# Kernel optimization log

Hardware: AMD Instinct MI355X
Metric: run time of the kernel (lower is better)

Reference implementation:

```python
import jax, jax.numpy as jnp
import numpy as np

B, N, D, H, MLP = 4, 1024, 1024, 16, 4096  # seq_len N must equal dim D; D = H * dim_head
DH = D // H
EPS = 1e-5


def layernorm(x, g, b):
    mu = jnp.mean(x, axis=-1, keepdims=True)
    var = jnp.var(x, axis=-1, keepdims=True)
    return (x - mu) * jax.lax.rsqrt(var + EPS) * g + b


def setup_inputs() -> dict:
    key = jax.random.key(0)
    ks = jax.random.split(key, 12)
    s = 0.02
    return {
        "x": jax.random.normal(ks[0], (B, N, D), jnp.float32),
        "enc_out": jax.random.normal(ks[1], (B, N, D), jnp.float32),
        # SelfAttention (heads=1, dim_head=D); weights stored (in, out) so we apply x @ W
        "sa_wq": jax.random.normal(ks[2], (D, D), jnp.float32) * s,
        "sa_wk": jax.random.normal(ks[3], (D, D), jnp.float32) * s,
        "sa_wv": jax.random.normal(ks[4], (D, D), jnp.float32) * s,
        "sa_g": jnp.ones((D,), jnp.float32),
        "sa_b": jnp.zeros((D,), jnp.float32),
        # CrossAttention
        "ca_wq": jax.random.normal(ks[5], (D, D), jnp.float32) * s,
        "ca_wk": jax.random.normal(ks[6], (D, D), jnp.float32) * s,
        "ca_wv": jax.random.normal(ks[7], (D, D), jnp.float32) * s,
        "ca_g": jnp.ones((D,), jnp.float32),
        "ca_b": jnp.zeros((D,), jnp.float32),
        # FeedForward
        "w1": jax.random.normal(ks[8], (D, MLP), jnp.float32) * s,
        "b1": jnp.zeros((MLP,), jnp.float32),
        "w2": jax.random.normal(ks[9], (MLP, D), jnp.float32) * s,
        "b2": jnp.zeros((D,), jnp.float32),
        "ff_g": jnp.ones((D,), jnp.float32),
        "ff_b": jnp.zeros((D,), jnp.float32),
    }


def reference(x, enc_out, sa_wq, sa_wk, sa_wv, sa_g, sa_b,
              ca_wq, ca_wk, ca_wv, ca_g, ca_b,
              w1, b1, w2, b2, ff_g, ff_b):
    b, n, d = x.shape
    # --- SelfAttention: heads=1, dim_head=dim -> scale = dim**-0.5 ---
    sa_scale = 1.0 / jnp.sqrt(jnp.asarray(d, x.dtype))
    q = x @ sa_wq
    k = x @ sa_wk
    v = x @ sa_wv
    dots = jnp.einsum('bid,bjd->bij', q, k) * sa_scale
    attn = jax.nn.softmax(dots, axis=-1)
    sa = jnp.einsum('bij,bjd->bid', attn, v)
    sa = layernorm(sa + x, sa_g, sa_b)

    # --- CrossAttention: Q . (K K^T) before softmax ---
    dh = d // H
    ca_scale = 1.0 / jnp.sqrt(jnp.asarray(dh, x.dtype))
    qc = sa @ ca_wq                                     # [b, n, d]; broadcast over heads
    kc = (enc_out @ ca_wk).reshape(b, n, H, dh).transpose(0, 2, 1, 3)  # [b, h, n, dh]
    vc = (enc_out @ ca_wv).reshape(b, n, H, dh).transpose(0, 2, 1, 3)
    kkt = jnp.einsum('bhid,bhjd->bhij', kc, kc) * ca_scale             # [b, h, n, n]
    dots = jnp.einsum('bid,bhjd->bhij', qc, kkt) * ca_scale            # q's d contracts kkt's last dim (n == d)
    attn = jax.nn.softmax(dots, axis=-1)
    out = jnp.einsum('bhij,bhjd->bhid', attn, vc)
    out = out.transpose(0, 2, 1, 3).reshape(b, n, d)
    ca = layernorm(out + enc_out, ca_g, ca_b)

    # --- FeedForward (dropout = identity in eval) ---
    h = jax.nn.gelu(ca @ w1 + b1, approximate=False) @ w2 + b2
    return layernorm(h + ca, ff_g, ff_b)
```

## Files before the change

### kernel.cpp

```cpp
#include <hip/hip_runtime.h>
#include <math.h>
#include <stdint.h>

typedef unsigned short u16;
typedef u16   u16x8 __attribute__((ext_vector_type(8)));
typedef __bf16 bf16x8 __attribute__((ext_vector_type(8)));
typedef float  f32x4 __attribute__((ext_vector_type(4)));

#define B_   4
#define N_   1024
#define D_   1024
#define MLP_ 4096

__device__ __forceinline__ float bf2f(u16 v) {
    unsigned u = ((unsigned)v) << 16;
    return __builtin_bit_cast(float, u);
}
__device__ __forceinline__ u16 f2bf(float f) {
    unsigned u = __builtin_bit_cast(unsigned, f);
    u += 0x7fff + ((u >> 16) & 1);
    return (u16)(u >> 16);
}
__device__ __forceinline__ bf16x8 ld8(const u16* p) {
    return __builtin_bit_cast(bf16x8, *(const u16x8*)p);
}
__device__ __forceinline__ void gll16(const u16* g, u16* l) {
    __builtin_amdgcn_global_load_lds(
        (const __attribute__((address_space(1))) unsigned int*)g,
        (__attribute__((address_space(3))) unsigned int*)l,
        16, 0, 0);
}
__device__ __forceinline__ float gelu_f(float v) {
    float xs = v * 0.70710678118654752f;
    float ax = fabsf(xs);
    float t  = __builtin_amdgcn_rcpf(fmaf(0.3275911f, ax, 1.0f));
    float p  = fmaf(1.061405429f, t, -1.453152027f);
    p = fmaf(p, t, 1.421413741f);
    p = fmaf(p, t, -0.284496736f);
    p = fmaf(p, t, 0.254829592f);
    p *= t;
    float e = __expf(-ax * ax);
    float er = 1.0f - p * e;
    er = copysignf(er, xs);
    return 0.5f * v * (1.0f + er);
}

__global__ __launch_bounds__(256)
void prep_all(const float* __restrict__ x, const float* __restrict__ enc,
              u16* __restrict__ xB, u16* __restrict__ encB,
              const float* __restrict__ p0, const float* __restrict__ p1,
              const float* __restrict__ p2, const float* __restrict__ p3,
              const float* __restrict__ p4, const float* __restrict__ p5,
              u16* __restrict__ Wsa, u16* __restrict__ Wca)
{
    __shared__ u16 tile[32][33];
    int bid = blockIdx.x;
    if (bid < 4096) {
        const float* in = x; u16* out = xB;
        if (bid >= 2048) { in = enc; out = encB; bid -= 2048; }
        long i = (long)bid * 256 + threadIdx.x;
        f32x4 a = *(const f32x4*)&in[i * 8];
        f32x4 b = *(const f32x4*)&in[i * 8 + 4];
        u16x8 h;
        h[0] = f2bf(a[0]); h[1] = f2bf(a[1]); h[2] = f2bf(a[2]); h[3] = f2bf(a[3]);
        h[4] = f2bf(b[0]); h[5] = f2bf(b[1]); h[6] = f2bf(b[2]); h[7] = f2bf(b[3]);
        *(u16x8*)&out[i * 8] = h;
        return;
    }
    int sub = bid - 4096;
    const int z = sub >> 10;
    const int t2 = sub & 1023;
    const int bx = (t2 & 31) * 32, by = (t2 >> 5) * 32;
    const float* in = p0;
    if (z == 1) in = p1;
    else if (z == 2) in = p2;
    else if (z == 3) in = p3;
    else if (z == 4) in = p4;
    else if (z == 5) in = p5;
    u16* out = (z < 3) ? Wsa + (long)z * (1 << 20) : Wca + (long)(z - 3) * (1 << 20);
    const int tx = threadIdx.x & 31, ty = threadIdx.x >> 5;
#pragma unroll
    for (int i = ty; i < 32; i += 8)
        tile[i][tx] = f2bf(in[(long)(by + i) * 1024 + bx + tx]);
    __syncthreads();
#pragma unroll
    for (int i = ty; i < 32; i += 8)
        out[(long)(bx + i) * 1024 + by + tx] = tile[tx][i];
}

template<int TM, int TN, int BK, int OUTF32, int BIAS, int GELU>
__device__ __forceinline__ void gemm_body(
    const u16* __restrict__ A, const u16* __restrict__ Bt, char* __restrict__ Cp,
    const float* __restrict__ bias, float scale, int K,
    int lda, int ldb, int ldc, int m0, int n0)
{
    constexpr int MT = TM / 32, NT = TN / 32;
    constexpr int CPT = BK / 8;
    constexpr int RPP = 2048 / BK;
    constexpr int CMASK = (CPT - 1) & 7;
    __shared__ alignas(16) u16 As[2][TM * BK];
    __shared__ alignas(16) u16 Bs[2][TN * BK];
    const int t = threadIdx.x, lane = t & 63, w = t >> 6;
    const int wr = (w >> 1) * (TM / 2), wc = (w & 1) * (TN / 2);
    const int fr = lane & 15, fq = lane >> 4;
    f32x4 acc[MT][NT] = {};

    const int r0a = t / CPT;
    const int c0sw = ((t % CPT) ^ (r0a & CMASK)) * 8;
    auto stageA = [&](u16* dst, int k0) {
#pragma unroll
        for (int p = 0; p < TM / RPP; p++)
            gll16(A + (long)(m0 + p * RPP + r0a) * lda + k0 + c0sw, dst + p * 2048 + w * 512);
    };
    auto stageB = [&](u16* dst, int k0) {
#pragma unroll
        for (int p = 0; p < TN / RPP; p++)
            gll16(Bt + (long)(n0 + p * RPP + r0a) * ldb + k0 + c0sw, dst + p * 2048 + w * 512);
    };

    stageA(As[0], 0);
    stageB(Bs[0], 0);
    int cur = 0;
    for (int k0 = 0; k0 < K; k0 += BK) {
        __syncthreads();
        if (k0 + BK < K) {
            stageA(As[cur ^ 1], k0 + BK);
            stageB(Bs[cur ^ 1], k0 + BK);
        }
        const u16* as = As[cur];
        const u16* bs = Bs[cur];
#pragma unroll
        for (int kk = 0; kk < BK; kk += 32) {
            bf16x8 af[MT], bfv[NT];
#pragma unroll
            for (int mt = 0; mt < MT; mt++) {
                const int row = wr + mt * 16 + fr;
                af[mt] = ld8(&as[row * BK + ((((kk >> 3) + fq) ^ (row & CMASK)) << 3)]);
            }
#pragma unroll
            for (int nt = 0; nt < NT; nt++) {
                const int row = wc + nt * 16 + fr;
                bfv[nt] = ld8(&bs[row * BK + ((((kk >> 3) + fq) ^ (row & CMASK)) << 3)]);
            }
#pragma unroll
            for (int mt = 0; mt < MT; mt++)
#pragma unroll
                for (int nt = 0; nt < NT; nt++)
                    acc[mt][nt] = __builtin_amdgcn_mfma_f32_16x16x32_bf16(af[mt], bfv[nt], acc[mt][nt], 0, 0, 0);
        }
        cur ^= 1;
    }

#pragma unroll
    for (int nt = 0; nt < NT; nt++) {
        const int col = n0 + wc + nt * 16 + fr;
        float bv = 0.f;
        if (BIAS) bv = bias[col];
#pragma unroll
        for (int mt = 0; mt < MT; mt++) {
            const int rbase = m0 + wr + mt * 16 + fq * 4;
#pragma unroll
            for (int r = 0; r < 4; r++) {
                float v = acc[mt][nt][r] * scale;
                if (BIAS) v += bv;
                if (GELU) v = gelu_f(v);
                long idx = (long)(rbase + r) * ldc + col;
                if (OUTF32) ((float*)Cp)[idx] = v;
                else        ((u16*) Cp)[idx] = f2bf(v);
            }
        }
    }
}

template<int TM, int TN, int BK, int SEL, int OUTF32, int BIAS, int GELU>
__global__ __launch_bounds__(256, ((TM + TN >= 256) ? ((BK == 64) ? 2 : 4)
                                                    : ((BK == 64) ? 3 : 4)))
void gemm_a(const u16* __restrict__ A0, const u16* __restrict__ A1,
            const u16* __restrict__ B0, const u16* __restrict__ B1,
            void* __restrict__ C0v, void* __restrict__ C1v,
            const float* __restrict__ bias,
            float scale, int K,
            int lda, int ldb, int ldc,
            long sA, long sB, long sC)
{
    int by = blockIdx.y, bz = blockIdx.z;
    const u16* A = A0; const u16* Bt = B0; char* Cp = (char*)C0v;
    if (SEL == 1) {
        int half = gridDim.y >> 1;
        if (by >= half) { A = A1; Bt = B1; Cp = (char*)C1v; by -= half; }
    }
    A += bz * sA;  Bt += bz * sB;  Cp += bz * sC * (OUTF32 ? 4 : 2);
    gemm_body<TM, TN, BK, OUTF32, BIAS, GELU>(
        A, Bt, Cp, bias, scale, K, lda, ldb, ldc, blockIdx.x * TM, by * TN);
}

__global__ __launch_bounds__(256, 4)
void gemm_qkv4(const u16* __restrict__ xB,  const u16* __restrict__ Wq,
               const u16* __restrict__ Wk,  u16* __restrict__ qB,
               u16* __restrict__ kB,
               const u16* __restrict__ Wv,  const u16* __restrict__ Wvc,
               const u16* __restrict__ encB,
               u16* __restrict__ vTB, u16* __restrict__ vcTB)
{
    const long M1 = (long)N_ * D_;
    int bid = blockIdx.x;
    const u16* A; const u16* Bt; u16* C; int m0, n0;
    if (bid < 512) {
        int bx = bid & 31, by = bid >> 5;
        A = xB; m0 = bx * 128;
        if (by < 8) { Bt = Wq; C = qB; n0 = by * 128; }
        else        { Bt = Wk; C = kB; n0 = (by - 8) * 128; }
    } else {
        int sub = bid - 512;
        int bx = sub & 7, by = (sub >> 3) & 7, bz = sub >> 6;
        m0 = bx * 128; n0 = by * 128;
        if (bz < 4) { A = Wv;  Bt = xB   + (long)bz * M1;       C = vTB  + (long)bz * M1; }
        else        { A = Wvc; Bt = encB + (long)(bz - 4) * M1; C = vcTB + (long)(bz - 4) * M1; }
    }
    gemm_body<128, 128, 32, 0, 0, 0>(
        A, Bt, (char*)C, nullptr, 1.f, 1024, 1024, 1024, 1024, m0, n0);
}

template<int INF32>
__global__ __launch_bounds__(256)
void transpose_cast(const void* __restrict__ in, u16* __restrict__ out,
                    int R, int C, long sIn, long sOut)
{
    __shared__ u16 tile[32][33];
    const char* ip = (const char*)in + (long)blockIdx.z * sIn * (INF32 ? 4 : 2);
    u16*        op = out + (long)blockIdx.z * sOut;
    const int bx = blockIdx.x * 32, by = blockIdx.y * 32;
    const int tx = threadIdx.x & 31, ty = threadIdx.x >> 5;
#pragma unroll
    for (int i = ty; i < 32; i += 8) {
        long idx = (long)(by + i) * C + bx + tx;
        tile[i][tx] = INF32 ? f2bf(((const float*)ip)[idx]) : ((const u16*)ip)[idx];
    }
    __syncthreads();
#pragma unroll
    for (int i = ty; i < 32; i += 8) op[(long)(bx + i) * R + by + tx] = tile[tx][i];
}

__global__ __launch_bounds__(256)
void transpose_ff(const float* __restrict__ w1, const float* __restrict__ w2,
                  u16* __restrict__ o1, u16* __restrict__ o2)
{
    __shared__ u16 tile[32][33];
    const float* in; u16* out; int R, C, bx, by;
    if (blockIdx.z == 0) {
        in = w1; out = o1; R = 1024; C = 4096;
        bx = blockIdx.x; by = blockIdx.y;
    } else {
        in = w2; out = o2; R = 4096; C = 1024;
        bx = blockIdx.x >> 2; by = blockIdx.y * 4 + (blockIdx.x & 3);
    }
    const int x0 = bx * 32, y0 = by * 32;
    const int tx = threadIdx.x & 31, ty = threadIdx.x >> 5;
#pragma unroll
    for (int i = ty; i < 32; i += 8)
        tile[i][tx] = f2bf(in[(long)(y0 + i) * C + x0 + tx]);
    __syncthreads();
#pragma unroll
    for (int i = ty; i < 32; i += 8)
        out[(long)(x0 + i) * R + y0 + tx] = tile[tx][i];
}

__global__ __launch_bounds__(256)
void softmax_1024(const float* __restrict__ in, u16* __restrict__ out)
{
    const int lane = threadIdx.x & 63, wv = threadIdx.x >> 6;
    const long row = (long)blockIdx.x * 4 + wv;
    const float* p = in + row * 1024 + lane * 16;
    float v[16];
#pragma unroll
    for (int q = 0; q < 4; q++) {
        f32x4 a = *(const f32x4*)(p + q * 4);
#pragma unroll
        for (int e = 0; e < 4; e++) v[q * 4 + e] = a[e];
    }
    float mx = v[0];
#pragma unroll
    for (int i = 1; i < 16; i++) mx = fmaxf(mx, v[i]);
#pragma unroll
    for (int off = 32; off; off >>= 1) mx = fmaxf(mx, __shfl_xor(mx, off, 64));
    float s = 0.f;
#pragma unroll
    for (int i = 0; i < 16; i++) { v[i] = __expf(v[i] - mx); s += v[i]; }
#pragma unroll
    for (int off = 32; off; off >>= 1) s += __shfl_xor(s, off, 64);
    const float inv = 1.0f / s;
    u16* qp = out + row * 1024 + lane * 16;
#pragma unroll
    for (int q = 0; q < 2; q++) {
        u16x8 o;
#pragma unroll
        for (int e = 0; e < 8; e++) o[e] = f2bf(v[q * 8 + e] * inv);
        *(u16x8*)(qp + q * 8) = o;
    }
}

template<int AF32, int RESF32, int OUTF32>
__global__ __launch_bounds__(256)
void ln_res(const void* __restrict__ Av, const void* __restrict__ Rv,
            const float* __restrict__ g, const float* __restrict__ be,
            void* __restrict__ out)
{
    const int lane = threadIdx.x & 63, wv = threadIdx.x >> 6;
    const long row = (long)blockIdx.x * 4 + wv;
    const long off = row * 1024 + lane * 16;
    const int c0 = lane * 16;
    float v[16];
    if (AF32) {
#pragma unroll
        for (int q = 0; q < 4; q++) {
            f32x4 a = *((const f32x4*)((const float*)Av + off) + q);
#pragma unroll
            for (int e = 0; e < 4; e++) v[q * 4 + e] = a[e];
        }
    } else {
#pragma unroll
        for (int q = 0; q < 2; q++) {
            u16x8 a = *((const u16x8*)((const u16*)Av + off) + q);
#pragma unroll
            for (int e = 0; e < 8; e++) v[q * 8 + e] = bf2f(a[e]);
        }
    }
    if (RESF32) {
#pragma unroll
        for (int q = 0; q < 4; q++) {
            f32x4 a = *((const f32x4*)((const float*)Rv + off) + q);
#pragma unroll
            for (int e = 0; e < 4; e++) v[q * 4 + e] += a[e];
        }
    } else {
#pragma unroll
        for (int q = 0; q < 2; q++) {
            u16x8 a = *((const u16x8*)((const u16*)Rv + off) + q);
#pragma unroll
            for (int e = 0; e < 8; e++) v[q * 8 + e] += bf2f(a[e]);
        }
    }
    float s = 0.f;
#pragma unroll
    for (int i = 0; i < 16; i++) s += v[i];
#pragma unroll
    for (int o = 32; o; o >>= 1) s += __shfl_xor(s, o, 64);
    const float mu = s * (1.f / 1024.f);
    float s2 = 0.f;
#pragma unroll
    for (int i = 0; i < 16; i++) { float d = v[i] - mu; s2 += d * d; }
#pragma unroll
    for (int o = 32; o; o >>= 1) s2 += __shfl_xor(s2, o, 64);
    const float rs = rsqrtf(s2 * (1.f / 1024.f) + 1e-5f);

    float ov[16];
#pragma unroll
    for (int q = 0; q < 4; q++) {
        f32x4 gv = *(const f32x4*)&g[c0 + q * 4];
        f32x4 bv = *(const f32x4*)&be[c0 + q * 4];
#pragma unroll
        for (int e = 0; e < 4; e++)
            ov[q * 4 + e] = (v[q * 4 + e] - mu) * rs * gv[e] + bv[e];
    }
    if (OUTF32) {
#pragma unroll
        for (int q = 0; q < 4; q++) {
            f32x4 o;
#pragma unroll
            for (int e = 0; e < 4; e++) o[e] = ov[q * 4 + e];
            *((f32x4*)((float*)out + off) + q) = o;
        }
    } else {
#pragma unroll
        for (int q = 0; q < 2; q++) {
            u16x8 o;
#pragma unroll
            for (int e = 0; e < 8; e++) o[e] = f2bf(ov[q * 8 + e]);
            *((u16x8*)((u16*)out + off) + q) = o;
        }
    }
}

__global__ __launch_bounds__(256, 3)
void flash_ca(const u16* __restrict__ P, const u16* __restrict__ Kc,
              const u16* __restrict__ VT, u16* __restrict__ O)
{
    __shared__ alignas(16) u16 Ks[2][64 * 64];
    __shared__ alignas(16) u16 Vs[2][64 * 64];
    __shared__ alignas(16) u16 Ps[128 * 72];
    const int b = blockIdx.z, h = blockIdx.y, it = blockIdx.x;
    const long base = (long)b * N_ * D_;
    const int t = threadIdx.x, lane = t & 63, w = t >> 6;
    const int fr = lane & 15, fq = lane >> 4;

    bf16x8 qf[2][2];
#pragma unroll
    for (int mt = 0; mt < 2; mt++)
#pragma unroll
        for (int hf = 0; hf < 2; hf++)
            qf[mt][hf] = ld8(&P[base + (long)(it * 128 + w * 32 + mt * 16 + fr) * D_
                                + h * 64 + hf * 32 + fq * 8]);

    const int svr = t >> 3, svc = ((t & 7) ^ (svr & 7)) * 8;
    auto stageK = [&](int buf, int jt) {
#pragma unroll
        for (int p = 0; p < 2; p++)
            gll16(Kc + base + (long)(jt * 64 + p * 32 + svr) * D_ + h * 64 + svc,
                  &Ks[buf][p * 2048 + w * 512]);
    };
    auto stageV = [&](int buf, int jt) {
#pragma unroll
        for (int p = 0; p < 2; p++)
            gll16(VT + base + (long)(h * 64 + p * 32 + svr) * D_ + jt * 64 + svc,
                  &Vs[buf][p * 2048 + w * 512]);
    };

    f32x4 o[2][4] = {};
    float l_lane[2][4] = {};

    stageK(0, 0); stageV(0, 0);
    int cur = 0;
    for (int jt = 0; jt < 16; jt++) {
        __syncthreads();
        if (jt + 1 < 16) { stageK(cur ^ 1, jt + 1); stageV(cur ^ 1, jt + 1); }
        const u16* ks = Ks[cur];
        const u16* vs = Vs[cur];

        f32x4 st[2][4] = {};
        __builtin_amdgcn_s_setprio(1);
#pragma unroll
        for (int nt = 0; nt < 4; nt++) {
            const int row = nt * 16 + fr;
            bf16x8 b0 = ld8(&ks[row * 64 + ((fq ^ (row & 7)) << 3)]);
            bf16x8 b1 = ld8(&ks[row * 64 + (((fq + 4) ^ (row & 7)) << 3)]);
#pragma unroll
            for (int mt = 0; mt < 2; mt++) {
                st[mt][nt] = __builtin_amdgcn_mfma_f32_16x16x32_bf16(qf[mt][0], b0, st[mt][nt], 0, 0, 0);
                st[mt][nt] = __builtin_amdgcn_mfma_f32_16x16x32_bf16(qf[mt][1], b1, st[mt][nt], 0, 0, 0);
            }
        }
        __builtin_amdgcn_s_setprio(0);
#pragma unroll
        for (int mt = 0; mt < 2; mt++)
#pragma unroll
            for (int nt = 0; nt < 4; nt++)
#pragma unroll
                for (int r = 0; r < 4; r++) {
                    float e = __expf(st[mt][nt][r]);
                    l_lane[mt][r] += e;
                    Ps[(w * 32 + mt * 16 + fq * 4 + r) * 72 + nt * 16 + fr] = f2bf(e);
                }
        __asm__ volatile("s_waitcnt lgkmcnt(0)" ::: "memory");
        bf16x8 vf[4][2];
#pragma unroll
        for (int dt = 0; dt < 4; dt++) {
            const int row = dt * 16 + fr;
            vf[dt][0] = ld8(&vs[row * 64 + ((fq ^ (row & 7)) << 3)]);
            vf[dt][1] = ld8(&vs[row * 64 + (((fq + 4) ^ (row & 7)) << 3)]);
        }
        __builtin_amdgcn_s_setprio(1);
#pragma unroll
        for (int mt = 0; mt < 2; mt++) {
            bf16x8 p0 = ld8(&Ps[(w * 32 + mt * 16 + fr) * 72 + fq * 8]);
            bf16x8 p1 = ld8(&Ps[(w * 32 + mt * 16 + fr) * 72 + 32 + fq * 8]);
#pragma unroll
            for (int dt = 0; dt < 4; dt++) {
                o[mt][dt] = __builtin_amdgcn_mfma_f32_16x16x32_bf16(p0, vf[dt][0], o[mt][dt], 0, 0, 0);
                o[mt][dt] = __builtin_amdgcn_mfma_f32_16x16x32_bf16(p1, vf[dt][1], o[mt][dt], 0, 0, 0);
            }
        }
        __builtin_amdgcn_s_setprio(0);
        cur ^= 1;
    }
#pragma unroll
    for (int mt = 0; mt < 2; mt++)
#pragma unroll
        for (int r = 0; r < 4; r++) {
            float lt = l_lane[mt][r];
#pragma unroll
            for (int off = 1; off < 16; off <<= 1) lt += __shfl_xor(lt, off, 64);
            l_lane[mt][r] = 1.0f / lt;
        }
#pragma unroll
    for (int mt = 0; mt < 2; mt++)
#pragma unroll
        for (int dt = 0; dt < 4; dt++)
#pragma unroll
            for (int r = 0; r < 4; r++)
                O[base + (long)(it * 128 + w * 32 + mt * 16 + fq * 4 + r) * D_
                  + h * 64 + dt * 16 + fr] = f2bf(o[mt][dt][r] * l_lane[mt][r]);
}

extern "C" void kernel_launch(void* const* d_in, const int* in_sizes, int n_in,
                              void* d_out, int out_size, void* d_ws, size_t ws_size,
                              hipStream_t stream)
{
    const float* x     = (const float*)d_in[0];
    const float* enc   = (const float*)d_in[1];
    const float* sa_wq = (const float*)d_in[2];
    const float* sa_wk = (const float*)d_in[3];
    const float* sa_wv = (const float*)d_in[4];
    const float* sa_g  = (const float*)d_in[5];
    const float* sa_b  = (const float*)d_in[6];
    const float* ca_wq = (const float*)d_in[7];
    const float* ca_wk = (const float*)d_in[8];
    const float* ca_wv = (const float*)d_in[9];
    const float* ca_g  = (const float*)d_in[10];
    const float* ca_b  = (const float*)d_in[11];
    const float* w1    = (const float*)d_in[12];
    const float* b1    = (const float*)d_in[13];
    const float* w2    = (const float*)d_in[14];
    const float* b2    = (const float*)d_in[15];
    const float* ff_g  = (const float*)d_in[16];
    const float* ff_b  = (const float*)d_in[17];

    char* ws = (char*)d_ws;
    const size_t MB = 1ull << 20;
    u16*  xB    = (u16*)(ws + 0 * MB);
    u16*  attnB = (u16*)(ws + 0 * MB);
    u16*  w2T   = (u16*)(ws + 0 * MB);
    u16*  encB  = (u16*)(ws + 8 * MB);
    u16*  w1T   = (u16*)(ws + 8 * MB);
    u16*  Wsa   = (u16*)(ws + 16 * MB);
    u16*  Wca   = (u16*)(ws + 22 * MB);
    float* h2F  = (float*)(ws + 16 * MB);
    u16*  qBsa  = (u16*)(ws + 28 * MB);
    u16*  E     = (u16*)(ws + 28 * MB);
    u16*  kBsa  = (u16*)(ws + 36 * MB);
    u16*  qBca  = (u16*)(ws + 36 * MB);
    u16*  calnB = (u16*)(ws + 36 * MB);
    u16*  vTB   = (u16*)(ws + 44 * MB);
    u16*  kBca  = (u16*)(ws + 44 * MB);
    u16*  h1B   = (u16*)(ws + 44 * MB);
    u16*  vcTB  = (u16*)(ws + 52 * MB);
    float* scF  = (float*)(ws + 60 * MB);
    u16*  kcT   = (u16*)(ws + 60 * MB);

    const dim3 blk(256, 1, 1);
    const long M1 = (long)N_ * D_;
    const long W1M = (long)1024 * 1024;

    prep_all<<<dim3(10240, 1, 1), blk, 0, stream>>>(
        x, enc, xB, encB, sa_wq, sa_wk, sa_wv, ca_wq, ca_wk, ca_wv, Wsa, Wca);

    gemm_qkv4<<<dim3(1024, 1, 1), blk, 0, stream>>>(
        xB, Wsa, Wsa + W1M, qBsa, kBsa,
        Wsa + 2 * W1M, Wca + 2 * W1M, encB, vTB, vcTB);
    gemm_a<128,64,64,0,1,0,0><<<dim3(8, 16, 4), blk, 0, stream>>>(
        qBsa, nullptr, kBsa, nullptr, scF, nullptr, nullptr,
        0.03125f, 1024, 1024, 1024, 1024, M1, M1, M1);
    softmax_1024<<<dim3(1024, 1, 1), blk, 0, stream>>>(scF, attnB);
    gemm_a<128,64,64,0,1,0,0><<<dim3(8, 16, 4), blk, 0, stream>>>(
        attnB, nullptr, vTB, nullptr, scF, nullptr, nullptr,
        1.f, 1024, 1024, 1024, 1024, M1, M1, M1);
    ln_res<1,1,0><<<dim3(1024, 1, 1), blk, 0, stream>>>(scF, x, sa_g, sa_b, E);

    gemm_a<128,128,64,1,0,0,0><<<dim3(32, 16, 1), blk, 0, stream>>>(
        E, encB, Wca, Wca + W1M, qBca, kBca, nullptr,
        1.f, 1024, 1024, 1024, 1024, 0, 0, 0);
    transpose_cast<0><<<dim3(32, 32, 4), blk, 0, stream>>>(kBca, kcT, 1024, 1024, M1, M1);
    gemm_a<128,64,64,0,0,0,0><<<dim3(8, 16, 4), blk, 0, stream>>>(
        qBca, nullptr, kcT, nullptr, attnB, nullptr, nullptr,
        0.015625f, 1024, 1024, 1024, 1024, M1, M1, M1);
    flash_ca<<<dim3(8, 16, 4), blk, 0, stream>>>(attnB, kBca, vcTB, E);
    ln_res<0,1,0><<<dim3(1024, 1, 1), blk, 0, stream>>>(E, enc, ca_g, ca_b, calnB);

    transpose_ff<<<dim3(128, 32, 2), blk, 0, stream>>>(w1, w2, w1T, w2T);
    gemm_a<128,128,32,0,0,1,1><<<dim3(32, 32, 1), blk, 0, stream>>>(
        calnB, nullptr, w1T, nullptr, h1B, nullptr, b1,
        1.f, 1024, 1024, 1024, 4096, 0, 0, 0);
    gemm_a<128,64,64,0,1,1,0><<<dim3(32, 16, 1), blk, 0, stream>>>(
        h1B, nullptr, w2T, nullptr, h2F, nullptr, b2,
        1.f, 4096, 4096, 4096, 1024, 0, 0, 0);
    ln_res<1,0,1><<<dim3(1024, 1, 1), blk, 0, stream>>>(h2F, calnB, ff_g, ff_b, (float*)d_out);
}
```

Baseline: 460.3 us.

## Fuse kc transpose into projection epilogue and split-K FF2 with atomics

The cross-attention K projection now writes a transposed bf16 copy of its output directly from the GEMM epilogue, which removes the separate transpose_cast kernel. The second feed-forward GEMM is split four ways along K with 128x128 tiles and accumulates into a zeroed fp32 buffer using atomicAdd. The bias b2 moves into the final layernorm kernel. This gives the FF2 GEMM more blocks to fill the GPU, at the cost of a 16MB memset, atomic traffic, and order-dependent float summation.

```diff
diff --git a/kernel.cpp b/kernel.cpp
--- a/kernel.cpp
+++ b/kernel.cpp
@@ -3,6 +3,7 @@
 #include <stdint.h>
 
 typedef unsigned short u16;
+typedef u16   u16x4 __attribute__((ext_vector_type(4)));
 typedef u16   u16x8 __attribute__((ext_vector_type(8)));
 typedef __bf16 bf16x8 __attribute__((ext_vector_type(8)));
 typedef float  f32x4 __attribute__((ext_vector_type(4)));
@@ -88,10 +89,10 @@
         out[(long)(bx + i) * 1024 + by + tx] = tile[tx][i];
 }
 
-template<int TM, int TN, int BK, int OUTF32, int BIAS, int GELU>
+template<int TM, int TN, int BK, int OUTF32, int BIAS, int GELU, int ATOMIC, int WT>
 __device__ __forceinline__ void gemm_body(
     const u16* __restrict__ A, const u16* __restrict__ Bt, char* __restrict__ Cp,
-    const float* __restrict__ bias, float scale, int K,
+    const float* __restrict__ bias, u16* __restrict__ CT, float scale, int K,
     int lda, int ldb, int ldc, int m0, int n0)
 {
     constexpr int MT = TM / 32, NT = TN / 32;
@@ -159,39 +160,48 @@
 #pragma unroll
         for (int mt = 0; mt < MT; mt++) {
             const int rbase = m0 + wr + mt * 16 + fq * 4;
+            u16 tv[4];
 #pragma unroll
             for (int r = 0; r < 4; r++) {
                 float v = acc[mt][nt][r] * scale;
                 if (BIAS) v += bv;
                 if (GELU) v = gelu_f(v);
                 long idx = (long)(rbase + r) * ldc + col;
-                if (OUTF32) ((float*)Cp)[idx] = v;
-                else        ((u16*) Cp)[idx] = f2bf(v);
+                if (ATOMIC)      atomicAdd((float*)Cp + idx, v);
+                else if (OUTF32) ((float*)Cp)[idx] = v;
+                else             ((u16*) Cp)[idx] = f2bf(v);
+                if (WT) tv[r] = f2bf(v);
             }
-        }
-    }
-}
-
-template<int TM, int TN, int BK, int SEL, int OUTF32, int BIAS, int GELU>
+            if (WT && CT) {
+                long tb = ((long)(rbase >> 10)) * 1048576 + (long)col * 1024 + (rbase & 1023);
+                *(u16x4*)&CT[tb] = *(const u16x4*)tv;
+            }
+        }
+    }
+}
+
+template<int TM, int TN, int BK, int SEL, int OUTF32, int BIAS, int GELU, int ATOMIC, int WT>
 __global__ __launch_bounds__(256, ((TM + TN >= 256) ? ((BK == 64) ? 2 : 4)
                                                     : ((BK == 64) ? 3 : 4)))
 void gemm_a(const u16* __restrict__ A0, const u16* __restrict__ A1,
             const u16* __restrict__ B0, const u16* __restrict__ B1,
             void* __restrict__ C0v, void* __restrict__ C1v,
-            const float* __restrict__ bias,
+            const float* __restrict__ bias, u16* __restrict__ CT,
             float scale, int K,
             int lda, int ldb, int ldc,
             long sA, long sB, long sC)
 {
     int by = blockIdx.y, bz = blockIdx.z;
     const u16* A = A0; const u16* Bt = B0; char* Cp = (char*)C0v;
+    u16* CTp = nullptr;
     if (SEL == 1) {
         int half = gridDim.y >> 1;
-        if (by >= half) { A = A1; Bt = B1; Cp = (char*)C1v; by -= half; }
+        if (by >= half) { A = A1; Bt = B1; Cp = (char*)C1v; by -= half; CTp = CT; }
     }
     A += bz * sA;  Bt += bz * sB;  Cp += bz * sC * (OUTF32 ? 4 : 2);
-    gemm_body<TM, TN, BK, OUTF32, BIAS, GELU>(
-        A, Bt, Cp, bias, scale, K, lda, ldb, ldc, blockIdx.x * TM, by * TN);
+    if (SEL == 3) { A += (long)bz * 1024; Bt += (long)bz * 1024; }
+    gemm_body<TM, TN, BK, OUTF32, BIAS, GELU, ATOMIC, WT>(
+        A, Bt, Cp, bias, CTp, scale, K, lda, ldb, ldc, blockIdx.x * TM, by * TN);
 }
 
 __global__ __launch_bounds__(256, 4)
@@ -217,28 +227,8 @@
         if (bz < 4) { A = Wv;  Bt = xB   + (long)bz * M1;       C = vTB  + (long)bz * M1; }
         else        { A = Wvc; Bt = encB + (long)(bz - 4) * M1; C = vcTB + (long)(bz - 4) * M1; }
     }
-    gemm_body<128, 128, 32, 0, 0, 0>(
-        A, Bt, (char*)C, nullptr, 1.f, 1024, 1024, 1024, 1024, m0, n0);
-}
-
-template<int INF32>
-__global__ __launch_bounds__(256)
-void transpose_cast(const void* __restrict__ in, u16* __restrict__ out,
-                    int R, int C, long sIn, long sOut)
-{
-    __shared__ u16 tile[32][33];
-    const char* ip = (const char*)in + (long)blockIdx.z * sIn * (INF32 ? 4 : 2);
-    u16*        op = out + (long)blockIdx.z * sOut;
-    const int bx = blockIdx.x * 32, by = blockIdx.y * 32;
-    const int tx = threadIdx.x & 31, ty = threadIdx.x >> 5;
-#pragma unroll
-    for (int i = ty; i < 32; i += 8) {
-        long idx = (long)(by + i) * C + bx + tx;
-        tile[i][tx] = INF32 ? f2bf(((const float*)ip)[idx]) : ((const u16*)ip)[idx];
-    }
-    __syncthreads();
-#pragma unroll
-    for (int i = ty; i < 32; i += 8) op[(long)(bx + i) * R + by + tx] = tile[tx][i];
+    gemm_body<128, 128, 32, 0, 0, 0, 0, 0>(
+        A, Bt, (char*)C, nullptr, nullptr, 1.f, 1024, 1024, 1024, 1024, m0, n0);
 }
 
 __global__ __launch_bounds__(256)
@@ -299,11 +289,11 @@
     }
 }
 
-template<int AF32, int RESF32, int OUTF32>
+template<int AF32, int RESF32, int OUTF32, int ADDB>
 __global__ __launch_bounds__(256)
 void ln_res(const void* __restrict__ Av, const void* __restrict__ Rv,
             const float* __restrict__ g, const float* __restrict__ be,
-            void* __restrict__ out)
+            void* __restrict__ out, const float* __restrict__ bb)
 {
     const int lane = threadIdx.x & 63, wv = threadIdx.x >> 6;
     const long row = (long)blockIdx.x * 4 + wv;
@@ -323,6 +313,14 @@
             u16x8 a = *((const u16x8*)((const u16*)Av + off) + q);
 #pragma unroll
             for (int e = 0; e < 8; e++) v[q * 8 + e] = bf2f(a[e]);
+        }
+    }
+    if (ADDB) {
+#pragma unroll
+        for (int q = 0; q < 4; q++) {
+            f32x4 a = *(const f32x4*)&bb[c0 + q * 4];
+#pragma unroll
+            for (int e = 0; e < 4; e++) v[q * 4 + e] += a[e];
         }
     }
     if (RESF32) {
@@ -546,31 +544,31 @@
     gemm_qkv4<<<dim3(1024, 1, 1), blk, 0, stream>>>(
         xB, Wsa, Wsa + W1M, qBsa, kBsa,
         Wsa + 2 * W1M, Wca + 2 * W1M, encB, vTB, vcTB);
-    gemm_a<128,64,64,0,1,0,0><<<dim3(8, 16, 4), blk, 0, stream>>>(
-        qBsa, nullptr, kBsa, nullptr, scF, nullptr, nullptr,
+    gemm_a<128,64,64,0,1,0,0,0,0><<<dim3(8, 16, 4), blk, 0, stream>>>(
+        qBsa, nullptr, kBsa, nullptr, scF, nullptr, nullptr, nullptr,
         0.03125f, 1024, 1024, 1024, 1024, M1, M1, M1);
     softmax_1024<<<dim3(1024, 1, 1), blk, 0, stream>>>(scF, attnB);
-    gemm_a<128,64,64,0,1,0,0><<<dim3(8, 16, 4), blk, 0, stream>>>(
-        attnB, nullptr, vTB, nullptr, scF, nullptr, nullptr,
+    gemm_a<128,64,64,0,1,0,0,0,0><<<dim3(8, 16, 4), blk, 0, stream>>>(
+        attnB, nullptr, vTB, nullptr, scF, nullptr, nullptr, nullptr,
         1.f, 1024, 1024, 1024, 1024, M1, M1, M1);
-    ln_res<1,1,0><<<dim3(1024, 1, 1), blk, 0, stream>>>(scF, x, sa_g, sa_b, E);
-
-    gemm_a<128,128,64,1,0,0,0><<<dim3(32, 16, 1), blk, 0, stream>>>(
-        E, encB, Wca, Wca + W1M, qBca, kBca, nullptr,
+    ln_res<1,1,0,0><<<dim3(1024, 1, 1), blk, 0, stream>>>(scF, x, sa_g, sa_b, E, nullptr);
+
+    gemm_a<128,128,64,1,0,0,0,0,1><<<dim3(32, 16, 1), blk, 0, stream>>>(
+        E, encB, Wca, Wca + W1M, qBca, kBca, nullptr, kcT,
         1.f, 1024, 1024, 1024, 1024, 0, 0, 0);
-    transpose_cast<0><<<dim3(32, 32, 4), blk, 0, stream>>>(kBca, kcT, 1024, 1024, M1, M1);
-    gemm_a<128,64,64,0,0,0,0><<<dim3(8, 16, 4), blk, 0, stream>>>(
-        qBca, nullptr, kcT, nullptr, attnB, nullptr, nullptr,
+    gemm_a<128,64,64,0,0,0,0,0,0><<<dim3(8, 16, 4), blk, 0, stream>>>(
+        qBca, nullptr, kcT, nullptr, attnB, nullptr, nullptr, nullptr,
         0.015625f, 1024, 1024, 1024, 1024, M1, M1, M1);
     flash_ca<<<dim3(8, 16, 4), blk, 0, stream>>>(attnB, kBca, vcTB, E);
-    ln_res<0,1,0><<<dim3(1024, 1, 1), blk, 0, stream>>>(E, enc, ca_g, ca_b, calnB);
-
+    ln_res<0,1,0,0><<<dim3(1024, 1, 1), blk, 0, stream>>>(E, enc, ca_g, ca_b, calnB, nullptr);
+
+    hipMemsetAsync(h2F, 0, (size_t)16 * MB, stream);
     transpose_ff<<<dim3(128, 32, 2), blk, 0, stream>>>(w1, w2, w1T, w2T);
-    gemm_a<128,128,32,0,0,1,1><<<dim3(32, 32, 1), blk, 0, stream>>>(
-        calnB, nullptr, w1T, nullptr, h1B, nullptr, b1,
+    gemm_a<128,128,32,0,0,1,1,0,0><<<dim3(32, 32, 1), blk, 0, stream>>>(
+        calnB, nullptr, w1T, nullptr, h1B, nullptr, b1, nullptr,
         1.f, 1024, 1024, 1024, 4096, 0, 0, 0);
-    gemm_a<128,64,64,0,1,1,0><<<dim3(32, 16, 1), blk, 0, stream>>>(
-        h1B, nullptr, w2T, nullptr, h2F, nullptr, b2,
-        1.f, 4096, 4096, 4096, 1024, 0, 0, 0);
-    ln_res<1,0,1><<<dim3(1024, 1, 1), blk, 0, stream>>>(h2F, calnB, ff_g, ff_b, (float*)d_out);
-}
+    gemm_a<128,128,32,3,1,0,0,1,0><<<dim3(32, 8, 4), blk, 0, stream>>>(
+        h1B, nullptr, w2T, nullptr, h2F, nullptr, nullptr, nullptr,
+        1.f, 1024, 4096, 4096, 1024, 0, 0, 0);
+    ln_res<1,0,1,1><<<dim3(1024, 1, 1), blk, 0, stream>>>(h2F, calnB, ff_g, ff_b, (float*)d_out, b2);
+}
```

Result: slower. 486.1 us (+5.6%).

## Use 256x256 GEMM for FF1 and split-K FF2 with bf16 partials

Applied to the files above, without the earlier changes.

Adds a dedicated 512-thread FF1 kernel with 256x256 tiles, swizzled LDS, double buffering and interleaved MFMA/load scheduling with priority hints, fusing bias and GELU. FF2 is split along K into two halves writing bf16 partials, which the final layernorm sums together with the bias. The aim is more reuse per tile in FF1 and more blocks in FF2. In exchange, the FF2 partial sums are rounded to bf16 before being added, which loses precision, and the FF1 epilogue writes scalar strided stores.

```diff
diff --git a/kernel.cpp b/kernel.cpp
--- a/kernel.cpp
+++ b/kernel.cpp
@@ -3,6 +3,7 @@
 #include <stdint.h>
 
 typedef unsigned short u16;
+typedef u16   u16x4 __attribute__((ext_vector_type(4)));
 typedef u16   u16x8 __attribute__((ext_vector_type(8)));
 typedef __bf16 bf16x8 __attribute__((ext_vector_type(8)));
 typedef float  f32x4 __attribute__((ext_vector_type(4)));
@@ -192,6 +193,130 @@
     A += bz * sA;  Bt += bz * sB;  Cp += bz * sC * (OUTF32 ? 4 : 2);
     gemm_body<TM, TN, BK, OUTF32, BIAS, GELU>(
         A, Bt, Cp, bias, scale, K, lda, ldb, ldc, blockIdx.x * TM, by * TN);
+}
+
+__global__ __launch_bounds__(512, 2)
+void gemm_ff1(const u16* __restrict__ A, const u16* __restrict__ Bt,
+              u16* __restrict__ C, const float* __restrict__ bias)
+{
+    __shared__ alignas(16) u16 As[2][256 * 64];
+    __shared__ alignas(16) u16 Bs[2][256 * 64];
+    const int m0 = blockIdx.x * 256, n0 = blockIdx.y * 256;
+    const int t = threadIdx.x, lane = t & 63, w = t >> 6;
+    const int wm = (w >> 2) * 128, wn = (w & 3) * 64;
+    const int fr = lane & 15, fq = lane >> 4;
+    f32x4 acc[8][4] = {};
+
+    const int r0a = t >> 3;
+    const int c0sw = ((t & 7) ^ (r0a & 7)) * 8;
+    auto stA = [&](u16* dst, int k0, int p) {
+        gll16(A + (long)(m0 + p * 64 + r0a) * 1024 + k0 + c0sw,
+              dst + p * 4096 + w * 512);
+    };
+    auto stB = [&](u16* dst, int k0, int p) {
+        gll16(Bt + (long)(n0 + p * 64 + r0a) * 1024 + k0 + c0sw,
+              dst + p * 4096 + w * 512);
+    };
+
+#pragma unroll
+    for (int p = 0; p < 4; p++) { stA(As[0], 0, p); stB(Bs[0], 0, p); }
+    __syncthreads();
+    int cur = 0;
+    for (int k0 = 0; k0 < 1024; k0 += 64) {
+        const u16* as = As[cur]; const u16* bs = Bs[cur];
+        u16* an = As[cur ^ 1];  u16* bn = Bs[cur ^ 1];
+        const bool pre = (k0 + 64 < 1024);
+        const int kn = k0 + 64;
+        bf16x8 af[4][2], bfv[4][2];
+
+        if (pre) { stA(an, kn, 0); stA(an, kn, 1); stA(an, kn, 2); stA(an, kn, 3); }
+#pragma unroll
+        for (int mf = 0; mf < 4; mf++)
+#pragma unroll
+            for (int kk = 0; kk < 2; kk++) {
+                const int row = wm + mf * 16 + fr;
+                af[mf][kk] = ld8(&as[row * 64 + (((kk * 4 + fq) ^ (row & 7)) << 3)]);
+            }
+#pragma unroll
+        for (int nf = 0; nf < 2; nf++)
+#pragma unroll
+            for (int kk = 0; kk < 2; kk++) {
+                const int row = wn + nf * 16 + fr;
+                bfv[nf][kk] = ld8(&bs[row * 64 + (((kk * 4 + fq) ^ (row & 7)) << 3)]);
+            }
+        __builtin_amdgcn_s_setprio(1);
+#pragma unroll
+        for (int mf = 0; mf < 4; mf++)
+#pragma unroll
+            for (int nf = 0; nf < 2; nf++)
+#pragma unroll
+                for (int kk = 0; kk < 2; kk++)
+                    acc[mf][nf] = __builtin_amdgcn_mfma_f32_16x16x32_bf16(af[mf][kk], bfv[nf][kk], acc[mf][nf], 0, 0, 0);
+        __builtin_amdgcn_s_setprio(0);
+
+        if (pre) { stB(bn, kn, 0); stB(bn, kn, 1); stB(bn, kn, 2); stB(bn, kn, 3); }
+#pragma unroll
+        for (int nf = 2; nf < 4; nf++)
+#pragma unroll
+            for (int kk = 0; kk < 2; kk++) {
+                const int row = wn + nf * 16 + fr;
+                bfv[nf][kk] = ld8(&bs[row * 64 + (((kk * 4 + fq) ^ (row & 7)) << 3)]);
+            }
+        __builtin_amdgcn_s_setprio(1);
+#pragma unroll
+        for (int mf = 0; mf < 4; mf++)
+#pragma unroll
+            for (int nf = 2; nf < 4; nf++)
+#pragma unroll
+                for (int kk = 0; kk < 2; kk++)
+                    acc[mf][nf] = __builtin_amdgcn_mfma_f32_16x16x32_bf16(af[mf][kk], bfv[nf][kk], acc[mf][nf], 0, 0, 0);
+        __builtin_amdgcn_s_setprio(0);
+
+#pragma unroll
+        for (int mf = 0; mf < 4; mf++)
+#pragma unroll
+            for (int kk = 0; kk < 2; kk++) {
+                const int row = wm + 64 + mf * 16 + fr;
+                af[mf][kk] = ld8(&as[row * 64 + (((kk * 4 + fq) ^ (row & 7)) << 3)]);
+            }
+        __builtin_amdgcn_s_setprio(1);
+#pragma unroll
+        for (int mf = 0; mf < 4; mf++)
+#pragma unroll
+            for (int nf = 0; nf < 2; nf++)
+#pragma unroll
+                for (int kk = 0; kk < 2; kk++)
+                    acc[4 + mf][nf] = __builtin_amdgcn_mfma_f32_16x16x32_bf16(af[mf][kk], bfv[nf][kk], acc[4 + mf][nf], 0, 0, 0);
+        __builtin_amdgcn_s_setprio(0);
+
+        __builtin_amdgcn_s_setprio(1);
+#pragma unroll
+        for (int mf = 0; mf < 4; mf++)
+#pragma unroll
+            for (int nf = 2; nf < 4; nf++)
+#pragma unroll
+                for (int kk = 0; kk < 2; kk++)
+                    acc[4 + mf][nf] = __builtin_amdgcn_mfma_f32_16x16x32_bf16(af[mf][kk], bfv[nf][kk], acc[4 + mf][nf], 0, 0, 0);
+        __builtin_amdgcn_s_setprio(0);
+
+        __syncthreads();
+        cur ^= 1;
+    }
+
+#pragma unroll
+    for (int nf = 0; nf < 4; nf++) {
+        const int col = n0 + wn + nf * 16 + fr;
+        const float bv = bias[col];
+#pragma unroll
+        for (int mf = 0; mf < 8; mf++) {
+            const int rbase = m0 + wm + mf * 16 + fq * 4;
+#pragma unroll
+            for (int r = 0; r < 4; r++) {
+                float v = gelu_f(acc[mf][nf][r] + bv);
+                C[(long)(rbase + r) * 4096 + col] = f2bf(v);
+            }
+        }
+    }
 }
 
 __global__ __launch_bounds__(256, 4)
@@ -299,11 +424,12 @@
     }
 }
 
-template<int AF32, int RESF32, int OUTF32>
+template<int AF32, int RESF32, int OUTF32, int ADDB, int A2>
 __global__ __launch_bounds__(256)
 void ln_res(const void* __restrict__ Av, const void* __restrict__ Rv,
             const float* __restrict__ g, const float* __restrict__ be,
-            void* __restrict__ out)
+            void* __restrict__ out, const float* __restrict__ bb,
+            const u16* __restrict__ Av2)
 {
     const int lane = threadIdx.x & 63, wv = threadIdx.x >> 6;
     const long row = (long)blockIdx.x * 4 + wv;
@@ -323,6 +449,22 @@
             u16x8 a = *((const u16x8*)((const u16*)Av + off) + q);
 #pragma unroll
             for (int e = 0; e < 8; e++) v[q * 8 + e] = bf2f(a[e]);
+        }
+    }
+    if (A2) {
+#pragma unroll
+        for (int q = 0; q < 2; q++) {
+            u16x8 a = *((const u16x8*)(Av2 + off) + q);
+#pragma unroll
+            for (int e = 0; e < 8; e++) v[q * 8 + e] += bf2f(a[e]);
+        }
+    }
+    if (ADDB) {
+#pragma unroll
+        for (int q = 0; q < 4; q++) {
+            f32x4 a = *(const f32x4*)&bb[c0 + q * 4];
+#pragma unroll
+            for (int e = 0; e < 4; e++) v[q * 4 + e] += a[e];
         }
     }
     if (RESF32) {
@@ -523,7 +665,7 @@
     u16*  w1T   = (u16*)(ws + 8 * MB);
     u16*  Wsa   = (u16*)(ws + 16 * MB);
     u16*  Wca   = (u16*)(ws + 22 * MB);
-    float* h2F  = (float*)(ws + 16 * MB);
+    u16*  h2P   = (u16*)(ws + 16 * MB);
     u16*  qBsa  = (u16*)(ws + 28 * MB);
     u16*  E     = (u16*)(ws + 28 * MB);
     u16*  kBsa  = (u16*)(ws + 36 * MB);
@@ -553,7 +695,8 @@
     gemm_a<128,64,64,0,1,0,0><<<dim3(8, 16, 4), blk, 0, stream>>>(
         attnB, nullptr, vTB, nullptr, scF, nullptr, nullptr,
         1.f, 1024, 1024, 1024, 1024, M1, M1, M1);
-    ln_res<1,1,0><<<dim3(1024, 1, 1), blk, 0, stream>>>(scF, x, sa_g, sa_b, E);
+    ln_res<1,1,0,0,0><<<dim3(1024, 1, 1), blk, 0, stream>>>(
+        scF, x, sa_g, sa_b, E, nullptr, nullptr);
 
     gemm_a<128,128,64,1,0,0,0><<<dim3(32, 16, 1), blk, 0, stream>>>(
         E, encB, Wca, Wca + W1M, qBca, kBca, nullptr,
@@ -563,14 +706,15 @@
         qBca, nullptr, kcT, nullptr, attnB, nullptr, nullptr,
         0.015625f, 1024, 1024, 1024, 1024, M1, M1, M1);
     flash_ca<<<dim3(8, 16, 4), blk, 0, stream>>>(attnB, kBca, vcTB, E);
-    ln_res<0,1,0><<<dim3(1024, 1, 1), blk, 0, stream>>>(E, enc, ca_g, ca_b, calnB);
+    ln_res<0,1,0,0,0><<<dim3(1024, 1, 1), blk, 0, stream>>>(
+        E, enc, ca_g, ca_b, calnB, nullptr, nullptr);
 
     transpose_ff<<<dim3(128, 32, 2), blk, 0, stream>>>(w1, w2, w1T, w2T);
-    gemm_a<128,128,32,0,0,1,1><<<dim3(32, 32, 1), blk, 0, stream>>>(
-        calnB, nullptr, w1T, nullptr, h1B, nullptr, b1,
-        1.f, 1024, 1024, 1024, 4096, 0, 0, 0);
-    gemm_a<128,64,64,0,1,1,0><<<dim3(32, 16, 1), blk, 0, stream>>>(
-        h1B, nullptr, w2T, nullptr, h2F, nullptr, b2,
-        1.f, 4096, 4096, 4096, 1024, 0, 0, 0);
-    ln_res<1,0,1><<<dim3(1024, 1, 1), blk, 0, stream>>>(h2F, calnB, ff_g, ff_b, (float*)d_out);
-}
+    gemm_ff1<<<dim3(16, 16, 1), dim3(512, 1, 1), 0, stream>>>(
+        calnB, w1T, h1B, b1);
+    gemm_a<128,128,32,0,0,0,0><<<dim3(32, 8, 2), blk, 0, stream>>>(
+        h1B, nullptr, w2T, nullptr, h2P, nullptr, nullptr,
+        1.f, 2048, 4096, 4096, 1024, 2048, 2048, 4194304);
+    ln_res<0,0,1,1,1><<<dim3(1024, 1, 1), blk, 0, stream>>>(
+        h2P, calnB, ff_g, ff_b, (float*)d_out, b2, h2P + 4194304);
+}
```

After: 458.3 us. About the same (-0.4%).
